# Performance work log

Hardware: AMD Instinct MI355X
Metric: run time of the kernel (lower is better)

Reference implementation:

```python
import jax, jax.numpy as jnp
import numpy as np
from jax.scipy.stats import norm

N_TOK, D_MODEL, N_EXP, N_SEL = 16384, 4096, 16, 4
NOISE_EPS = 0.01
LOSS_LAMBDA = 0.01


def setup_inputs() -> dict:
    key = jax.random.key(0)
    kx, k1, k2, kn, kz = jax.random.split(key, 5)
    x = jax.random.normal(kx, (N_TOK, D_MODEL), dtype=jnp.float32)
    w1 = jax.random.normal(k1, (N_EXP, D_MODEL), dtype=jnp.float32) * 0.02
    w2 = jax.random.normal(k2, (N_EXP, N_EXP), dtype=jnp.float32) * 0.02
    wn = jax.random.normal(kn, (N_EXP, D_MODEL), dtype=jnp.float32) * 0.02
    noise = jax.random.normal(kz, (N_TOK, N_EXP), dtype=jnp.float32)
    return {"x": x, "w1": w1, "w2": w2, "wn": wn, "noise": noise}


def _cv_squared(v, eps=1e-10):
    # torch .var() is unbiased (ddof=1)
    return jnp.var(v, ddof=1) / (jnp.mean(v) ** 2 + eps)


def reference(x, w1, w2, wn, noise):
    # MLP gate: Linear(D->E, no bias) -> tanh -> Linear(E->E, no bias)
    logits_gate = jnp.einsum("te,fe->tf", jnp.tanh(jnp.einsum("td,ed->te", x, w1)), w2)
    noise_control = jax.nn.softplus(jnp.einsum("td,ed->te", x, wn)) + NOISE_EPS
    logits_noise = noise * noise_control
    logits = logits_gate + logits_noise  # [T, E]

    m = min(N_SEL + 1, N_EXP)  # k+1 values for threshold computation
    top_logits, top_indices = jax.lax.top_k(logits, m)  # [T, m]
    top_k_logits = top_logits[:, :N_SEL]
    top_k_indices = top_indices[:, :N_SEL]
    top_k_scores = jax.nn.softmax(top_k_logits, axis=1)  # [T, k]

    # importance: scatter top-k scores back to dense [T, E]
    rows = jnp.arange(N_TOK)[:, None]
    scores_filtered = jnp.zeros_like(logits).at[rows, top_k_indices].set(top_k_scores)
    importance = scores_filtered.sum(0)  # [E]

    # load: smooth estimator via Normal CDF (faithful to source, which
    # compares logits_noise against the in/out thresholds)
    threshold_if_in = top_logits[:, N_SEL:N_SEL + 1]       # (k+1)-th top value, [T,1]
    threshold_if_out = top_logits[:, N_SEL - 1:N_SEL]      # k-th top value, [T,1]
    is_in = logits_noise > threshold_if_in
    prob_if_in = norm.cdf((logits_gate - threshold_if_in) / noise_control)
    prob_if_out = norm.cdf((logits_gate - threshold_if_out) / noise_control)
    prob = jnp.where(is_in, prob_if_in, prob_if_out)
    load = prob.sum(0)  # [E]

    gate_loss = LOSS_LAMBDA * (_cv_squared(importance) + _cv_squared(load))
    return top_k_indices, top_k_scores, gate_loss
```

## Files before the change

### kernel.cpp

```cpp
#include <hip/hip_runtime.h>
#include <math.h>

#define N_TOK   16384
#define D_MODEL 4096
#define N_EXP   16
#define N_SEL   4
#define WELEM   (N_EXP * D_MODEL)

typedef __bf16 bf16x8 __attribute__((ext_vector_type(8)));
typedef float  f32x4  __attribute__((ext_vector_type(4)));

#define MFMA(a, b, c) __builtin_amdgcn_mfma_f32_16x16x32_bf16((a), (b), (c), 0, 0, 0)

__global__ __launch_bounds__(256) void wprep_kernel(const float* __restrict__ w1,
                                                    const float* __restrict__ wn,
                                                    __bf16* __restrict__ wbuf)
{
    const int i = blockIdx.x * 256 + threadIdx.x;
    {
        const float v = w1[i];
        const __bf16 h = (__bf16)v;  const float r1 = v - (float)h;
        const __bf16 m = (__bf16)r1; const float r2 = r1 - (float)m;
        wbuf[i] = h; wbuf[WELEM + i] = m; wbuf[2 * WELEM + i] = (__bf16)r2;
    }
    {
        const float v = wn[i];
        const __bf16 h = (__bf16)v;  const float r1 = v - (float)h;
        const __bf16 m = (__bf16)r1; const float r2 = r1 - (float)m;
        wbuf[3 * WELEM + i] = h; wbuf[4 * WELEM + i] = m; wbuf[5 * WELEM + i] = (__bf16)r2;
    }
}

__global__ __launch_bounds__(256) void gate_kernel(
    const float* __restrict__ x, const __bf16* __restrict__ wbuf,
    const float* __restrict__ w2, const float* __restrict__ noise,
    float* __restrict__ out, float* __restrict__ g_imp, float* __restrict__ g_load)
{
    __shared__ float red[4][16][32];
    __shared__ float dsum[16][32];
    __shared__ float s_imp[N_EXP], s_ld[N_EXP];

    const int tid  = threadIdx.x;
    const int lane = tid & 63;
    const int wv   = tid >> 6;
    const int ml   = lane & 15;
    const int q    = lane >> 4;
    const int t0   = blockIdx.x * 16;

    const __bf16* w1h = wbuf;
    const __bf16* w1m = wbuf + WELEM;
    const __bf16* w1l = wbuf + 2 * WELEM;
    const __bf16* wnh = wbuf + 3 * WELEM;
    const __bf16* wnm = wbuf + 4 * WELEM;
    const __bf16* wnl = wbuf + 5 * WELEM;

    const size_t xoff = (size_t)(t0 + ml) * D_MODEL + wv * 1024 + q * 8;
    const int    woff = ml * D_MODEL + wv * 1024 + q * 8;

    f32x4 c1 = {0.f, 0.f, 0.f, 0.f};
    f32x4 c2 = {0.f, 0.f, 0.f, 0.f};

    #pragma unroll 2
    for (int it = 0; it < 32; ++it) {
        const int ko = it * 32;
        const float4 xa = *(const float4*)(x + xoff + ko);
        const float4 xb = *(const float4*)(x + xoff + ko + 4);
        const bf16x8 a1h = *(const bf16x8*)(w1h + woff + ko);
        const bf16x8 a1m = *(const bf16x8*)(w1m + woff + ko);
        const bf16x8 a1l = *(const bf16x8*)(w1l + woff + ko);
        const bf16x8 a2h = *(const bf16x8*)(wnh + woff + ko);
        const bf16x8 a2m = *(const bf16x8*)(wnm + woff + ko);
        const bf16x8 a2l = *(const bf16x8*)(wnl + woff + ko);

        const float xv[8] = {xa.x, xa.y, xa.z, xa.w, xb.x, xb.y, xb.z, xb.w};
        bf16x8 xh, xm8, xl;
        #pragma unroll
        for (int j = 0; j < 8; ++j) {
            const float v  = xv[j];
            const __bf16 h = (__bf16)v;   const float r1 = v - (float)h;
            const __bf16 md = (__bf16)r1; const float r2 = r1 - (float)md;
            xh[j] = h; xm8[j] = md; xl[j] = (__bf16)r2;
        }

        c1 = MFMA(a1h, xh, c1);  c1 = MFMA(a1h, xm8, c1); c1 = MFMA(a1m, xh, c1);
        c1 = MFMA(a1h, xl, c1);  c1 = MFMA(a1l, xh, c1);  c1 = MFMA(a1m, xm8, c1);
        c2 = MFMA(a2h, xh, c2);  c2 = MFMA(a2h, xm8, c2); c2 = MFMA(a2m, xh, c2);
        c2 = MFMA(a2h, xl, c2);  c2 = MFMA(a2l, xh, c2);  c2 = MFMA(a2m, xm8, c2);
    }

    #pragma unroll
    for (int r = 0; r < 4; ++r) {
        red[wv][ml][q * 4 + r]      = c1[r];
        red[wv][ml][16 + q * 4 + r] = c2[r];
    }
    __syncthreads();

    for (int idx = tid; idx < 512; idx += 256) {
        const int tk = idx >> 5, o = idx & 31;
        dsum[tk][o] = red[0][tk][o] + red[1][tk][o] + red[2][tk][o] + red[3][tk][o];
    }
    if (tid < N_EXP) { s_imp[tid] = 0.f; s_ld[tid] = 0.f; }
    __syncthreads();

    if (tid < 16) {
        const int t = t0 + tid;
        float dot[32];
        #pragma unroll
        for (int e = 0; e < 32; ++e) dot[e] = dsum[tid][e];

        float th[N_EXP], nc[N_EXP];
        #pragma unroll
        for (int e = 0; e < N_EXP; ++e) th[e] = tanhf(dot[e]);
        #pragma unroll
        for (int e = 0; e < N_EXP; ++e) {
            const float v = dot[N_EXP + e];
            nc[e] = fmaxf(v, 0.f) + log1pf(expf(-fabsf(v))) + 0.01f;
        }

        float lg[N_EXP];
        #pragma unroll
        for (int f = 0; f < N_EXP; ++f) {
            float s = 0.f;
            #pragma unroll
            for (int e = 0; e < N_EXP; ++e) s = fmaf(th[e], w2[f * 16 + e], s);
            lg[f] = s;
        }

        float ln[N_EXP], v[N_EXP];
        {
            const float4* nz = (const float4*)(noise + (size_t)t * 16);
            const float4 n0 = nz[0], n1 = nz[1], n2 = nz[2], n3 = nz[3];
            const float nzv[16] = {n0.x, n0.y, n0.z, n0.w, n1.x, n1.y, n1.z, n1.w,
                                   n2.x, n2.y, n2.z, n2.w, n3.x, n3.y, n3.z, n3.w};
            #pragma unroll
            for (int e = 0; e < N_EXP; ++e) {
                ln[e] = nzv[e] * nc[e];
                v[e]  = lg[e] + ln[e];
            }
        }

        float tv[5]; int ti[5];
        #pragma unroll
        for (int j = 0; j < 5; ++j) {
            float best = -INFINITY; int bi = 0;
            #pragma unroll
            for (int e = 0; e < N_EXP; ++e) {
                bool taken = false;
                #pragma unroll
                for (int jj = 0; jj < 5; ++jj)
                    if (jj < j) taken = taken || (ti[jj] == e);
                if (!taken && v[e] > best) { best = v[e]; bi = e; }
            }
            tv[j] = best; ti[j] = bi;
        }

        const float mx = tv[0];
        float ex[4], ssum = 0.f;
        #pragma unroll
        for (int j = 0; j < 4; ++j) { ex[j] = expf(tv[j] - mx); ssum += ex[j]; }
        const float inv = 1.f / ssum;
        float sc[4];
        #pragma unroll
        for (int j = 0; j < 4; ++j) sc[j] = ex[j] * inv;

        #pragma unroll
        for (int j = 0; j < 4; ++j) atomicAdd(&s_imp[ti[j]], sc[j]);

        const float thr_in = tv[4], thr_out = tv[3];
        #pragma unroll
        for (int e = 0; e < N_EXP; ++e) {
            const bool  is_in = ln[e] > thr_in;
            const float thr   = is_in ? thr_in : thr_out;
            const float z     = (lg[e] - thr) / nc[e];
            const float prob  = 0.5f * (1.f + erff(z * 0.70710678118654752f));
            atomicAdd(&s_ld[e], prob);
        }

        ((float4*)out)[t] = make_float4((float)ti[0], (float)ti[1],
                                        (float)ti[2], (float)ti[3]);
        ((float4*)(out + N_TOK * N_SEL))[t] = make_float4(sc[0], sc[1], sc[2], sc[3]);
    }
    __syncthreads();
    if (tid < N_EXP)            atomicAdd(&g_imp[tid], s_imp[tid]);
    else if (tid < 2 * N_EXP)   atomicAdd(&g_load[tid - N_EXP], s_ld[tid - N_EXP]);
}

__global__ void loss_kernel(const float* __restrict__ g_imp,
                            const float* __restrict__ g_load,
                            float* __restrict__ out)
{
    if (threadIdx.x == 0 && blockIdx.x == 0) {
        double mi = 0.0, ml = 0.0;
        for (int e = 0; e < N_EXP; ++e) { mi += g_imp[e]; ml += g_load[e]; }
        mi /= N_EXP; ml /= N_EXP;
        double vi = 0.0, vl = 0.0;
        for (int e = 0; e < N_EXP; ++e) {
            const double di = g_imp[e] - mi;  vi += di * di;
            const double dl = g_load[e] - ml; vl += dl * dl;
        }
        vi /= (N_EXP - 1); vl /= (N_EXP - 1);
        const double ci = vi / (mi * mi + 1e-10);
        const double cl = vl / (ml * ml + 1e-10);
        out[N_TOK * N_SEL * 2] = (float)(0.01 * (ci + cl));
    }
}

extern "C" void kernel_launch(void* const* d_in, const int* in_sizes, int n_in,
                              void* d_out, int out_size, void* d_ws, size_t ws_size,
                              hipStream_t stream)
{
    const float* x     = (const float*)d_in[0];
    const float* w1    = (const float*)d_in[1];
    const float* w2    = (const float*)d_in[2];
    const float* wn    = (const float*)d_in[3];
    const float* noise = (const float*)d_in[4];
    float* out = (float*)d_out;

    __bf16* wbuf  = (__bf16*)d_ws;
    float*  g_imp = (float*)((char*)d_ws + (1 << 20));
    float*  g_load = g_imp + N_EXP;

    hipMemsetAsync(g_imp, 0, 2 * N_EXP * sizeof(float), stream);

    wprep_kernel<<<WELEM / 256, 256, 0, stream>>>(w1, wn, wbuf);
    gate_kernel<<<N_TOK / 16, 256, 0, stream>>>(x, wbuf, w2, noise, out,
                                                g_imp, g_load);
    loss_kernel<<<1, 64, 0, stream>>>(g_imp, g_load, out);
}
```

Baseline: 436.8 us.

## Stage x tiles into LDS with async double-buffered loads, 64 tokens per block

Each block now handles 64 tokens with one wave per 16-token group, and each wave runs the full reduction dimension. The x tiles are brought into LDS through asynchronous global-to-LDS loads with double buffering and an XOR swizzle. This removes the cross-wave partial-sum reduction and is meant to overlap x loads with MFMA compute. In exchange, the grid shrinks to a quarter of the waves and each wave's dependent MFMA chain becomes four times longer, which can reduce latency hiding.

```diff
diff --git a/kernel.cpp b/kernel.cpp
--- a/kernel.cpp
+++ b/kernel.cpp
@@ -11,6 +11,8 @@
 typedef float  f32x4  __attribute__((ext_vector_type(4)));
 
 #define MFMA(a, b, c) __builtin_amdgcn_mfma_f32_16x16x32_bf16((a), (b), (c), 0, 0, 0)
+#define AS1 __attribute__((address_space(1)))
+#define AS3 __attribute__((address_space(3)))
 
 __global__ __launch_bounds__(256) void wprep_kernel(const float* __restrict__ w1,
                                                     const float* __restrict__ wn,
@@ -31,21 +33,49 @@
     }
 }
 
-__global__ __launch_bounds__(256) void gate_kernel(
+__device__ __forceinline__ void stage_load(const float* __restrict__ x,
+                                           float4* xs, int buf, int w, int l,
+                                           int t0, int kbase)
+{
+    #pragma unroll
+    for (int j = 0; j < 8; ++j) {
+        const int tl     = j * 2 + (l >> 5);
+        const int k4slot = l & 31;
+        const int k4data = k4slot ^ tl;
+        const float* g = x + (size_t)(t0 + w * 16 + tl) * D_MODEL + kbase + k4data * 4;
+        float4* lbase = xs + buf * 2048 + w * 512 + j * 64;
+        __builtin_amdgcn_global_load_lds((const AS1 void*)(const void*)g,
+                                         (AS3 void*)(void*)lbase, 16, 0, 0);
+    }
+}
+
+__device__ __forceinline__ void split3(const float4 a, const float4 b,
+                                       bf16x8& h, bf16x8& m, bf16x8& lo)
+{
+    const float v[8] = {a.x, a.y, a.z, a.w, b.x, b.y, b.z, b.w};
+    #pragma unroll
+    for (int j = 0; j < 8; ++j) {
+        const __bf16 hh = (__bf16)v[j]; const float r1 = v[j] - (float)hh;
+        const __bf16 mm = (__bf16)r1;   const float r2 = r1 - (float)mm;
+        h[j] = hh; m[j] = mm; lo[j] = (__bf16)r2;
+    }
+}
+
+__global__ __launch_bounds__(256, 2) void gate_kernel(
     const float* __restrict__ x, const __bf16* __restrict__ wbuf,
     const float* __restrict__ w2, const float* __restrict__ noise,
     float* __restrict__ out, float* __restrict__ g_imp, float* __restrict__ g_load)
 {
-    __shared__ float red[4][16][32];
-    __shared__ float dsum[16][32];
+    __shared__ float4 xs[4096];
+    __shared__ float dsum[4][16][33];
     __shared__ float s_imp[N_EXP], s_ld[N_EXP];
 
-    const int tid  = threadIdx.x;
-    const int lane = tid & 63;
-    const int wv   = tid >> 6;
-    const int ml   = lane & 15;
-    const int q    = lane >> 4;
-    const int t0   = blockIdx.x * 16;
+    const int tid = threadIdx.x;
+    const int l   = tid & 63;
+    const int w   = tid >> 6;
+    const int ml  = l & 15;
+    const int q   = l >> 4;
+    const int t0  = blockIdx.x * 64;
 
     const __bf16* w1h = wbuf;
     const __bf16* w1m = wbuf + WELEM;
@@ -53,60 +83,56 @@
     const __bf16* wnh = wbuf + 3 * WELEM;
     const __bf16* wnm = wbuf + 4 * WELEM;
     const __bf16* wnl = wbuf + 5 * WELEM;
-
-    const size_t xoff = (size_t)(t0 + ml) * D_MODEL + wv * 1024 + q * 8;
-    const int    woff = ml * D_MODEL + wv * 1024 + q * 8;
+    const int woff = ml * D_MODEL + q * 8;
 
     f32x4 c1 = {0.f, 0.f, 0.f, 0.f};
     f32x4 c2 = {0.f, 0.f, 0.f, 0.f};
 
-    #pragma unroll 2
-    for (int it = 0; it < 32; ++it) {
-        const int ko = it * 32;
-        const float4 xa = *(const float4*)(x + xoff + ko);
-        const float4 xb = *(const float4*)(x + xoff + ko + 4);
-        const bf16x8 a1h = *(const bf16x8*)(w1h + woff + ko);
-        const bf16x8 a1m = *(const bf16x8*)(w1m + woff + ko);
-        const bf16x8 a1l = *(const bf16x8*)(w1l + woff + ko);
-        const bf16x8 a2h = *(const bf16x8*)(wnh + woff + ko);
-        const bf16x8 a2m = *(const bf16x8*)(wnm + woff + ko);
-        const bf16x8 a2l = *(const bf16x8*)(wnl + woff + ko);
-
-        const float xv[8] = {xa.x, xa.y, xa.z, xa.w, xb.x, xb.y, xb.z, xb.w};
-        bf16x8 xh, xm8, xl;
-        #pragma unroll
-        for (int j = 0; j < 8; ++j) {
-            const float v  = xv[j];
-            const __bf16 h = (__bf16)v;   const float r1 = v - (float)h;
-            const __bf16 md = (__bf16)r1; const float r2 = r1 - (float)md;
-            xh[j] = h; xm8[j] = md; xl[j] = (__bf16)r2;
-        }
-
-        c1 = MFMA(a1h, xh, c1);  c1 = MFMA(a1h, xm8, c1); c1 = MFMA(a1m, xh, c1);
-        c1 = MFMA(a1h, xl, c1);  c1 = MFMA(a1l, xh, c1);  c1 = MFMA(a1m, xm8, c1);
-        c2 = MFMA(a2h, xh, c2);  c2 = MFMA(a2h, xm8, c2); c2 = MFMA(a2m, xh, c2);
-        c2 = MFMA(a2h, xl, c2);  c2 = MFMA(a2l, xh, c2);  c2 = MFMA(a2m, xm8, c2);
+    stage_load(x, xs, 0, w, l, t0, 0);
+    if (tid < N_EXP) { s_imp[tid] = 0.f; s_ld[tid] = 0.f; }
+    __syncthreads();
+
+    for (int s = 0; s < 32; ++s) {
+        if (s < 31) stage_load(x, xs, (s + 1) & 1, w, l, t0, (s + 1) * 128);
+
+        const int kbase = s * 128;
+        const int xb    = (s & 1) * 2048 + w * 512 + ml * 32;
+        #pragma unroll
+        for (int step = 0; step < 4; ++step) {
+            const int kq = step * 8 + q * 2;
+            const float4 va = xs[xb + (kq ^ ml)];
+            const float4 vb = xs[xb + ((kq + 1) ^ ml)];
+            bf16x8 xh, xm, xl;
+            split3(va, vb, xh, xm, xl);
+
+            const int wo = woff + kbase + step * 32;
+            const bf16x8 a1h = *(const bf16x8*)(w1h + wo);
+            const bf16x8 a1m = *(const bf16x8*)(w1m + wo);
+            const bf16x8 a1l = *(const bf16x8*)(w1l + wo);
+            const bf16x8 a2h = *(const bf16x8*)(wnh + wo);
+            const bf16x8 a2m = *(const bf16x8*)(wnm + wo);
+            const bf16x8 a2l = *(const bf16x8*)(wnl + wo);
+
+            c1 = MFMA(a1h, xh, c1); c1 = MFMA(a1h, xm, c1); c1 = MFMA(a1m, xh, c1);
+            c1 = MFMA(a1h, xl, c1); c1 = MFMA(a1l, xh, c1); c1 = MFMA(a1m, xm, c1);
+            c2 = MFMA(a2h, xh, c2); c2 = MFMA(a2h, xm, c2); c2 = MFMA(a2m, xh, c2);
+            c2 = MFMA(a2h, xl, c2); c2 = MFMA(a2l, xh, c2); c2 = MFMA(a2m, xm, c2);
+        }
+        __syncthreads();
     }
 
     #pragma unroll
     for (int r = 0; r < 4; ++r) {
-        red[wv][ml][q * 4 + r]      = c1[r];
-        red[wv][ml][16 + q * 4 + r] = c2[r];
+        dsum[w][ml][q * 4 + r]      = c1[r];
+        dsum[w][ml][16 + q * 4 + r] = c2[r];
     }
     __syncthreads();
 
-    for (int idx = tid; idx < 512; idx += 256) {
-        const int tk = idx >> 5, o = idx & 31;
-        dsum[tk][o] = red[0][tk][o] + red[1][tk][o] + red[2][tk][o] + red[3][tk][o];
-    }
-    if (tid < N_EXP) { s_imp[tid] = 0.f; s_ld[tid] = 0.f; }
-    __syncthreads();
-
-    if (tid < 16) {
-        const int t = t0 + tid;
+    if (ml == l) {
+        const int t = t0 + w * 16 + ml;
         float dot[32];
         #pragma unroll
-        for (int e = 0; e < 32; ++e) dot[e] = dsum[tid][e];
+        for (int e = 0; e < 32; ++e) dot[e] = dsum[w][ml][e];
 
         float th[N_EXP], nc[N_EXP];
         #pragma unroll
@@ -216,14 +242,14 @@
     const float* noise = (const float*)d_in[4];
     float* out = (float*)d_out;
 
-    __bf16* wbuf  = (__bf16*)d_ws;
-    float*  g_imp = (float*)((char*)d_ws + (1 << 20));
+    __bf16* wbuf   = (__bf16*)d_ws;
+    float*  g_imp  = (float*)((char*)d_ws + (1 << 20));
     float*  g_load = g_imp + N_EXP;
 
     hipMemsetAsync(g_imp, 0, 2 * N_EXP * sizeof(float), stream);
 
     wprep_kernel<<<WELEM / 256, 256, 0, stream>>>(w1, wn, wbuf);
-    gate_kernel<<<N_TOK / 16, 256, 0, stream>>>(x, wbuf, w2, noise, out,
+    gate_kernel<<<N_TOK / 64, 256, 0, stream>>>(x, wbuf, w2, noise, out,
                                                 g_imp, g_load);
     loss_kernel<<<1, 64, 0, stream>>>(g_imp, g_load, out);
 }
```

Result: slower. 457.1 us (+4.6%).
